# Optimization experiments

Measured on AMD Instinct MI355X. Metric: run time of the kernel, lower is better.

## Reference

```python
import math
import jax, jax.numpy as jnp
import numpy as np

W_BITS = 8
A_BITS = 8
N_HEADS = 16

def fake_quant(x, bits):
    # symmetric per-tensor fake quantization with straight-through estimator
    if bits >= 32:
        return x
    qmax = float(2 ** (bits - 1) - 1)
    scale = jnp.maximum(jnp.max(jnp.abs(x)) / qmax, 1e-8)
    q = jnp.round(x / scale) * scale
    return x + jax.lax.stop_gradient(q - x)

def qlinear(x, W, b):
    # QuantizeLinear: quantize activations (a_bits) and weights (w_bits), then y = x @ W^T + b
    xq = fake_quant(x, A_BITS)
    Wq = fake_quant(W, W_BITS)
    return jnp.einsum('bsd,ed->bse', xq, Wq) + b

def setup_inputs() -> dict:
    key = jax.random.key(0)
    B, S, D = 2, 2048, 1024
    ks = jax.random.split(key, 6)
    inp = {
        'hidden_states': jax.random.normal(ks[0], (B, S, D), dtype=jnp.float32),
        'attention_mask': jnp.ones((B, S), dtype=jnp.float32),
        'Wq': 0.02 * jax.random.normal(ks[1], (D, D), dtype=jnp.float32),
        'bq': jnp.zeros((D,), dtype=jnp.float32),
        'Wk': 0.02 * jax.random.normal(ks[2], (D, D), dtype=jnp.float32),
        'bk': jnp.zeros((D,), dtype=jnp.float32),
        'Wv': 0.02 * jax.random.normal(ks[3], (D, D), dtype=jnp.float32),
        'bv': jnp.zeros((D,), dtype=jnp.float32),
        'Wo': 0.02 * jax.random.normal(ks[4], (D, D), dtype=jnp.float32),
        'bo': jnp.zeros((D,), dtype=jnp.float32),
    }
    return inp

def reference(hidden_states, attention_mask, Wq, bq, Wk, bk, Wv, bv, Wo, bo):
    B, S, D = hidden_states.shape
    H = N_HEADS
    hd = D // H

    q = qlinear(hidden_states, Wq, bq).reshape(B, S, H, hd)
    k = qlinear(hidden_states, Wk, bk).reshape(B, S, H, hd)
    v = qlinear(hidden_states, Wv, bv).reshape(B, S, H, hd)

    # scores: [B, H, Sq, Sk]
    scores = jnp.einsum('bqhd,bkhd->bhqk', q, k) / math.sqrt(hd)
    mask_bias = (1.0 - attention_mask)[:, None, None, :] * -10000.0
    scores = scores + mask_bias
    probs = jax.nn.softmax(scores, axis=-1)

    attn = jnp.einsum('bhqk,bkhd->bqhd', probs, v).reshape(B, S, D)
    return qlinear(attn, Wo, bo)
```

## Files before the change

### kernel.cpp

```cpp
#include <hip/hip_runtime.h>
#include <cstddef>
#include <cstdint>

constexpr int Bb = 2, Ss = 2048, Dd = 1024, Hh = 16, HD = 64;
constexpr int Mm = Bb * Ss;

typedef int v4i __attribute__((ext_vector_type(4)));
typedef __bf16 bf16x8 __attribute__((ext_vector_type(8)));
typedef float f32x16 __attribute__((ext_vector_type(16)));

#define QPOSTMUL 0.18033688f
#define MASKBIAS -14426.950408f

__device__ __forceinline__ float qscale(float amax) {
    return fmaxf(amax / 127.0f, 1e-8f);
}

__device__ __forceinline__ unsigned short bf16rtn(float x) {
    __bf16 b = (__bf16)x;
    return __builtin_bit_cast(unsigned short, b);
}

__device__ __forceinline__ unsigned pack_bf16x2(float a, float b) {
    unsigned ua = __float_as_uint(a), ub = __float_as_uint(b);
    unsigned ha = (ua + 0x7fffu + ((ua >> 16) & 1u)) >> 16;
    unsigned hb = (ub + 0x7fffu + ((ub >> 16) & 1u)) & 0xffff0000u;
    return ha | hb;
}

__global__ void amax_all(const float4* __restrict__ hidden,
                         const float4* __restrict__ w0, const float4* __restrict__ w1,
                         const float4* __restrict__ w2, const float4* __restrict__ w3,
                         unsigned* __restrict__ slots) {
    const float4* src; int n4, slot, bx, nb;
    if (blockIdx.x < 448) { src = hidden; n4 = Mm * Dd / 4; slot = 0; bx = blockIdx.x; nb = 448; }
    else {
        int w = (blockIdx.x - 448) >> 4; bx = (blockIdx.x - 448) & 15; nb = 16;
        src = w == 0 ? w0 : w == 1 ? w1 : w == 2 ? w2 : w3;
        n4 = Dd * Dd / 4; slot = 1 + w;
    }
    float m = 0.f;
    for (int i = bx * blockDim.x + threadIdx.x; i < n4; i += nb * blockDim.x) {
        float4 v = src[i];
        m = fmaxf(m, fmaxf(fmaxf(fabsf(v.x), fabsf(v.y)), fmaxf(fabsf(v.z), fabsf(v.w))));
    }
    #pragma unroll
    for (int off = 32; off > 0; off >>= 1) m = fmaxf(m, __shfl_down(m, off, 64));
    __shared__ float sm[4];
    int lane = threadIdx.x & 63, wid = threadIdx.x >> 6;
    if (lane == 0) sm[wid] = m;
    __syncthreads();
    if (threadIdx.x == 0) {
        float mm = fmaxf(fmaxf(sm[0], sm[1]), fmaxf(sm[2], sm[3]));
        atomicMax(slots + slot, __float_as_uint(mm));
    }
}

__global__ void quant_all(const float* __restrict__ hidden,
                          const float* __restrict__ w0, const float* __restrict__ w1,
                          const float* __restrict__ w2, const float* __restrict__ w3,
                          const float* __restrict__ amax,
                          char* __restrict__ hq8, char* __restrict__ Wall8) {
    const float* x; char* y; int n4, slot, bx, nb;
    if (blockIdx.x < 1024) { x = hidden; y = hq8; n4 = Mm * Dd / 4; slot = 0; bx = blockIdx.x; nb = 1024; }
    else {
        int w = (blockIdx.x - 1024) >> 5; bx = (blockIdx.x - 1024) & 31; nb = 32;
        x = w == 0 ? w0 : w == 1 ? w1 : w == 2 ? w2 : w3;
        y = Wall8 + ((size_t)w << 20);
        n4 = Dd * Dd / 4; slot = 1 + w;
    }
    float s = qscale(amax[slot]);
    const float4* x4 = (const float4*)x;
    char4* y4 = (char4*)y;
    for (int i = bx * blockDim.x + threadIdx.x; i < n4; i += nb * blockDim.x) {
        float4 v = x4[i];
        char4 q;
        q.x = (char)(int)rintf(v.x / s);
        q.y = (char)(int)rintf(v.y / s);
        q.z = (char)(int)rintf(v.z / s);
        q.w = (char)(int)rintf(v.w / s);
        y4[i] = q;
    }
}

__global__ void quant_a(const float* __restrict__ x, char* __restrict__ y,
                        const float* __restrict__ amax, int n4) {
    float s = qscale(amax[0]);
    int stride = gridDim.x * blockDim.x;
    const float4* x4 = (const float4*)x;
    char4* y4 = (char4*)y;
    for (int i = blockIdx.x * blockDim.x + threadIdx.x; i < n4; i += stride) {
        float4 v = x4[i];
        char4 q;
        q.x = (char)(int)rintf(v.x / s);
        q.y = (char)(int)rintf(v.y / s);
        q.z = (char)(int)rintf(v.z / s);
        q.w = (char)(int)rintf(v.w / s);
        y4[i] = q;
    }
}

#define GLOAD_LDS16(g, l) __builtin_amdgcn_global_load_lds( \
    (const __attribute__((address_space(1))) unsigned int*)(g), \
    (__attribute__((address_space(3))) unsigned int*)(l), 16, 0, 0)

__device__ __forceinline__ void gemm128_core(const char* __restrict__ A, const char* __restrict__ Bw,
                                             int bm, int bn, int K, int t,
                                             char* At, char* Bt, v4i acc[4][4]) {
    const int lane = t & 63, w = t >> 6;
    const int wm = (w >> 1) * 64, wn = (w & 1) * 64;
    const int lr = lane & 15, kq = lane >> 4;
    const int rs = w * 16 + (lane >> 2);
    const int cc = lane & 3;

    for (int k0 = 0; k0 < K; k0 += 64) {
        __syncthreads();
        #pragma unroll
        for (int h = 0; h < 2; h++) {
            int r = rs + h * 64;
            int cs = cc ^ ((r >> 1) & 3);
            GLOAD_LDS16(A  + (size_t)(bm + r) * K + k0 + cs * 16, At + r * 64 + cc * 16);
            GLOAD_LDS16(Bw + (size_t)(bn + r) * K + k0 + cs * 16, Bt + r * 64 + cc * 16);
        }
        __syncthreads();

        v4i af[4], bf[4];
        #pragma unroll
        for (int mt = 0; mt < 4; mt++) {
            int row = wm + mt * 16 + lr;
            af[mt] = *(const v4i*)(At + row * 64 + ((kq ^ ((row >> 1) & 3)) << 4));
        }
        #pragma unroll
        for (int nt = 0; nt < 4; nt++) {
            int row = wn + nt * 16 + lr;
            bf[nt] = *(const v4i*)(Bt + row * 64 + ((kq ^ ((row >> 1) & 3)) << 4));
        }
        #pragma unroll
        for (int mt = 0; mt < 4; mt++)
            #pragma unroll
            for (int nt = 0; nt < 4; nt++)
                acc[mt][nt] = __builtin_amdgcn_mfma_i32_16x16x64_i8(af[mt], bf[nt], acc[mt][nt], 0, 0, 0);
    }
}

__global__ __launch_bounds__(256) void gemm_qkv(const char* __restrict__ A,
                                                const char* __restrict__ Wall8,
                                                const float* __restrict__ bq,
                                                const float* __restrict__ bk,
                                                const float* __restrict__ bv,
                                                const float* __restrict__ amax,
                                                unsigned short* __restrict__ qb16,
                                                unsigned short* __restrict__ kb16,
                                                unsigned short* __restrict__ vt16) {
    __shared__ alignas(16) char At[128 * 64];
    __shared__ alignas(16) char Bt[128 * 64];
    const int t = threadIdx.x, lane = t & 63, w = t >> 6;
    const int mat = blockIdx.x >> 3;
    const int bn = (blockIdx.x & 7) * 128, bm = blockIdx.y * 128;
    const int wm = (w >> 1) * 64, wn = (w & 1) * 64;
    const int lr = lane & 15, kq = lane >> 4;

    const v4i vzero = {0, 0, 0, 0};
    v4i acc[4][4];
    #pragma unroll
    for (int mt = 0; mt < 4; mt++)
        #pragma unroll
        for (int nt = 0; nt < 4; nt++) acc[mt][nt] = vzero;

    const char* Bw = Wall8 + ((size_t)mat << 20);
    gemm128_core(A, Bw, bm, bn, Dd, t, At, Bt, acc);

    const float* bias = mat == 0 ? bq : mat == 1 ? bk : bv;
    float sc = qscale(amax[0]) * qscale(amax[1 + mat]);
    float pm = (mat == 0) ? QPOSTMUL : 1.0f;

    #pragma unroll
    for (int nt = 0; nt < 4; nt++) {
        int n = bn + wn + nt * 16 + lr;
        float bv_ = bias[n];
        #pragma unroll
        for (int mt = 0; mt < 4; mt++) {
            if (mat == 2) {
                int m0 = bm + wm + mt * 16 + kq * 4;
                int b_ = m0 >> 11, s_ = m0 & 2047;
                int e = n & 63, hc = n >> 6;
                ushort4 hv;
                hv.x = bf16rtn((float)acc[mt][nt][0] * sc + bv_);
                hv.y = bf16rtn((float)acc[mt][nt][1] * sc + bv_);
                hv.z = bf16rtn((float)acc[mt][nt][2] * sc + bv_);
                hv.w = bf16rtn((float)acc[mt][nt][3] * sc + bv_);
                size_t ad = (((size_t)(b_ * Hh + hc) * 64 + e) * Ss) + s_;
                *(ushort4*)(vt16 + ad) = hv;
            } else {
                unsigned short* C = mat == 0 ? qb16 : kb16;
                #pragma unroll
                for (int rg = 0; rg < 4; rg++) {
                    int m = bm + wm + mt * 16 + kq * 4 + rg;
                    C[(size_t)m * Dd + n] = bf16rtn(((float)acc[mt][nt][rg] * sc + bv_) * pm);
                }
            }
        }
    }
}

__global__ __launch_bounds__(256) void gemm_o(const char* __restrict__ A,
                                              const char* __restrict__ Bw,
                                              const float* __restrict__ bias,
                                              const float* __restrict__ amaxA,
                                              const float* __restrict__ amaxB,
                                              float* __restrict__ C) {
    __shared__ alignas(16) char At[128 * 64];
    __shared__ alignas(16) char Bt[64 * 64];
    const int t = threadIdx.x, lane = t & 63, w = t >> 6;
    const int bn = blockIdx.x * 64, bm = blockIdx.y * 128;
    const int wm = (w >> 1) * 64, wn = (w & 1) * 32;
    const int lr = lane & 15, kq = lane >> 4;
    const int rs = t >> 2, cc = t & 3;
    const int cs = cc ^ ((rs >> 1) & 3);
    const int rs2 = rs + 64, cs2 = cc ^ ((rs2 >> 1) & 3);

    const v4i vzero = {0, 0, 0, 0};
    v4i acc[4][2];
    #pragma unroll
    for (int mt = 0; mt < 4; mt++) { acc[mt][0] = vzero; acc[mt][1] = vzero; }

    for (int k0 = 0; k0 < Dd; k0 += 64) {
        __syncthreads();
        GLOAD_LDS16(A  + (size_t)(bm + rs)  * Dd + k0 + cs  * 16, At + rs  * 64 + cc * 16);
        GLOAD_LDS16(A  + (size_t)(bm + rs2) * Dd + k0 + cs2 * 16, At + rs2 * 64 + cc * 16);
        GLOAD_LDS16(Bw + (size_t)(bn + rs)  * Dd + k0 + cs  * 16, Bt + rs  * 64 + cc * 16);
        __syncthreads();

        v4i af[4], bf[2];
        #pragma unroll
        for (int mt = 0; mt < 4; mt++) {
            int row = wm + mt * 16 + lr;
            af[mt] = *(const v4i*)(At + row * 64 + ((kq ^ ((row >> 1) & 3)) << 4));
        }
        #pragma unroll
        for (int nt = 0; nt < 2; nt++) {
            int row = wn + nt * 16 + lr;
            bf[nt] = *(const v4i*)(Bt + row * 64 + ((kq ^ ((row >> 1) & 3)) << 4));
        }
        #pragma unroll
        for (int mt = 0; mt < 4; mt++)
            #pragma unroll
            for (int nt = 0; nt < 2; nt++)
                acc[mt][nt] = __builtin_amdgcn_mfma_i32_16x16x64_i8(af[mt], bf[nt], acc[mt][nt], 0, 0, 0);
    }

    float sc = qscale(amaxA[0]) * qscale(amaxB[0]);
    #pragma unroll
    for (int nt = 0; nt < 2; nt++) {
        int n = bn + wn + nt * 16 + lr;
        float bv_ = bias[n];
        #pragma unroll
        for (int mt = 0; mt < 4; mt++)
            #pragma unroll
            for (int rg = 0; rg < 4; rg++) {
                int m = bm + wm + mt * 16 + kq * 4 + rg;
                C[(size_t)m * Dd + n] = (float)acc[mt][nt][rg] * sc + bv_;
            }
    }
}

__global__ __launch_bounds__(256) void attn_mfma(
    const unsigned short* __restrict__ qb16, const unsigned short* __restrict__ kb16,
    const unsigned short* __restrict__ vt16,
    const float* __restrict__ mask, float* __restrict__ Ob, unsigned* __restrict__ amax_out) {
    __shared__ alignas(16) unsigned short KsHi[64][72], VsHi[64][72];
    __shared__ alignas(16) unsigned PwU[4][32][36];
    __shared__ float mbias[64];
    __shared__ float wred[4];

    const int t = threadIdx.x, lane = t & 63, wq = t >> 6;
    const int ln31 = lane & 31, h5 = lane >> 5;
    const int b = blockIdx.z, h = blockIdx.y, q0 = blockIdx.x * 128;

    bf16x8 qf[4];
    {
        int qrow = q0 + wq * 32 + ln31;
        const unsigned short* qb_ = qb16 + ((size_t)(b * Ss + qrow)) * Dd + h * 64 + h5 * 8;
        #pragma unroll
        for (int c = 0; c < 4; c++) qf[c] = *(const bf16x8*)(qb_ + c * 16);
    }

    const int srow = t >> 2, cp = (t & 3) * 2;
    const int rho = (srow >> 1) + (srow & 1) * 32;
    int4 pk0, pk1, pv0, pv1; float pmask = 1.f;
    auto prefetch = [&](int k0) {
        const unsigned short* gk = kb16 + ((size_t)(b * Ss + k0 + srow)) * Dd + h * 64 + cp * 8;
        const unsigned short* gv = vt16 + (((size_t)(b * Hh + h) * 64 + srow)) * Ss + k0 + cp * 8;
        pk0 = *(const int4*)gk; pk1 = *(const int4*)(gk + 8);
        pv0 = *(const int4*)gv; pv1 = *(const int4*)(gv + 8);
        if (t < 64) pmask = mask[b * Ss + k0 + t];
    };

    f32x16 o0 = 0.f, o1 = 0.f;
    float lp[16];
    #pragma unroll
    for (int r = 0; r < 16; r++) lp[r] = 0.f;

    prefetch(0);
    for (int k0 = 0; k0 < Ss; k0 += 64) {
        __syncthreads();
        *(int4*)&KsHi[rho][cp * 8]      = pk0;
        *(int4*)&KsHi[rho][cp * 8 + 8]  = pk1;
        *(int4*)&VsHi[srow][cp * 8]     = pv0;
        *(int4*)&VsHi[srow][cp * 8 + 8] = pv1;
        if (t < 64) mbias[t] = (1.0f - pmask) * MASKBIAS;
        __syncthreads();
        if (k0 + 64 < Ss) prefetch(k0 + 64);

        f32x16 sc0 = 0.f, sc1 = 0.f;
        #pragma unroll
        for (int c = 0; c < 4; c++) {
            bf16x8 kh0 = *(const bf16x8*)&KsHi[ln31][c * 16 + h5 * 8];
            bf16x8 kh1 = *(const bf16x8*)&KsHi[32 + ln31][c * 16 + h5 * 8];
            sc0 = __builtin_amdgcn_mfma_f32_32x32x16_bf16(qf[c], kh0, sc0, 0, 0, 0);
            sc1 = __builtin_amdgcn_mfma_f32_32x32x16_bf16(qf[c], kh1, sc1, 0, 0, 0);
        }

        float mb0 = mbias[2 * ln31], mb1 = mbias[2 * ln31 + 1];
        #pragma unroll
        for (int r = 0; r < 16; r++) {
            float p0 = __builtin_amdgcn_exp2f(sc0[r] + mb0);
            float p1 = __builtin_amdgcn_exp2f(sc1[r] + mb1);
            lp[r] += p0 + p1;
            int row = (r & 3) + 8 * (r >> 2) + 4 * h5;
            PwU[wq][row][ln31] = pack_bf16x2(p0, p1);
        }

        #pragma unroll
        for (int c = 0; c < 4; c++) {
            bf16x8 pf = *(const bf16x8*)((const unsigned short*)&PwU[wq][ln31][0] + c * 16 + h5 * 8);
            bf16x8 vh0 = *(const bf16x8*)&VsHi[ln31][c * 16 + h5 * 8];
            bf16x8 vh1 = *(const bf16x8*)&VsHi[32 + ln31][c * 16 + h5 * 8];
            o0 = __builtin_amdgcn_mfma_f32_32x32x16_bf16(pf, vh0, o0, 0, 0, 0);
            o1 = __builtin_amdgcn_mfma_f32_32x32x16_bf16(pf, vh1, o1, 0, 0, 0);
        }
    }

    float lmax = 0.f;
    #pragma unroll
    for (int r = 0; r < 16; r++) {
        float l = lp[r];
        #pragma unroll
        for (int off = 1; off < 32; off <<= 1) l += __shfl_xor(l, off, 32);
        float inv = 1.0f / l;
        int row = q0 + wq * 32 + (r & 3) + 8 * (r >> 2) + 4 * h5;
        size_t ro = ((size_t)(b * Ss + row)) * Dd + h * 64;
        float v0 = o0[r] * inv, v1 = o1[r] * inv;
        Ob[ro + ln31] = v0;
        Ob[ro + 32 + ln31] = v1;
        lmax = fmaxf(lmax, fmaxf(fabsf(v0), fabsf(v1)));
    }
    #pragma unroll
    for (int off = 32; off > 0; off >>= 1) lmax = fmaxf(lmax, __shfl_xor(lmax, off, 64));
    if (lane == 0) wred[wq] = lmax;
    __syncthreads();
    if (t == 0) {
        float m = fmaxf(fmaxf(wred[0], wred[1]), fmaxf(wred[2], wred[3]));
        atomicMax(amax_out, __float_as_uint(m));
    }
}

extern "C" void kernel_launch(void* const* d_in, const int* in_sizes, int n_in,
                              void* d_out, int out_size, void* d_ws, size_t ws_size,
                              hipStream_t stream) {
    const float* hidden = (const float*)d_in[0];
    const float* mask   = (const float*)d_in[1];
    const float* Wq = (const float*)d_in[2];
    const float* bq = (const float*)d_in[3];
    const float* Wk = (const float*)d_in[4];
    const float* bk = (const float*)d_in[5];
    const float* Wv = (const float*)d_in[6];
    const float* bv = (const float*)d_in[7];
    const float* Wo = (const float*)d_in[8];
    const float* bo = (const float*)d_in[9];
    float* out = (float*)d_out;

    char* ws = (char*)d_ws;
    float* scal = (float*)ws;
    size_t off = 1024;
    const size_t szH8 = (size_t)Mm * Dd;
    const size_t szHb = (size_t)Mm * Dd * sizeof(unsigned short);
    const size_t szHf = (size_t)Mm * Dd * sizeof(float);
    char* hq8   = ws + off; off += szH8;
    char* Wall8 = ws + off; off += 4u << 20;
    char* aq8   = ws + off; off += szH8;
    unsigned short* qb16 = (unsigned short*)(ws + off); off += szHb;
    unsigned short* kb16 = (unsigned short*)(ws + off); off += szHb;
    unsigned short* vt16 = (unsigned short*)(ws + off); off += szHb;
    float* ab = (float*)(ws + off); off += szHf;

    hipMemsetAsync(scal, 0, 64, stream);

    amax_all<<<512, 256, 0, stream>>>((const float4*)hidden, (const float4*)Wq,
                                      (const float4*)Wk, (const float4*)Wv, (const float4*)Wo,
                                      (unsigned*)scal);
    quant_all<<<1152, 256, 0, stream>>>(hidden, Wq, Wk, Wv, Wo, scal, hq8, Wall8);

    gemm_qkv<<<dim3(24, 32), 256, 0, stream>>>(hq8, Wall8, bq, bk, bv, scal,
                                               qb16, kb16, vt16);

    attn_mfma<<<dim3(Ss / 128, Hh, Bb), 256, 0, stream>>>(qb16, kb16, vt16,
                                                          mask, ab, (unsigned*)(scal + 5));

    quant_a<<<1024, 256, 0, stream>>>(ab, aq8, scal + 5, Mm * Dd / 4);

    gemm_o<<<dim3(16, 32), 256, 0, stream>>>(aq8, Wall8 + (3u << 20), bo,
                                             scal + 5, scal + 4, out);
}
```

Measured before the change: 237.8 us.

## Split attention key blocks across wave pairs with 64-query tiles and LDS reduction

The attention kernel now handles 64 queries per block instead of 128. Each pair of waves shares a 32-query slice and splits every 64-key tile in half, and their partial outputs and row sums are combined through a shared-memory buffer at the end. This doubles the grid size to raise occupancy and parallelism, and halves per-wave MFMA work per tile. In exchange, K/V tiles are loaded from global memory twice as often per query, and a final cross-wave reduction plus extra syncs are added. Shared memory is pooled and aliased so the reduction buffer reuses the K/V/P space.

```diff
diff --git a/kernel.cpp b/kernel.cpp
--- a/kernel.cpp
+++ b/kernel.cpp
@@ -19,13 +19,6 @@
 __device__ __forceinline__ unsigned short bf16rtn(float x) {
     __bf16 b = (__bf16)x;
     return __builtin_bit_cast(unsigned short, b);
-}
-
-__device__ __forceinline__ unsigned pack_bf16x2(float a, float b) {
-    unsigned ua = __float_as_uint(a), ub = __float_as_uint(b);
-    unsigned ha = (ua + 0x7fffu + ((ua >> 16) & 1u)) >> 16;
-    unsigned hb = (ub + 0x7fffu + ((ub >> 16) & 1u)) & 0xffff0000u;
-    return ha | hb;
 }
 
 __global__ void amax_all(const float4* __restrict__ hidden,
@@ -268,25 +261,29 @@
     const unsigned short* __restrict__ qb16, const unsigned short* __restrict__ kb16,
     const unsigned short* __restrict__ vt16,
     const float* __restrict__ mask, float* __restrict__ Ob, unsigned* __restrict__ amax_out) {
-    __shared__ alignas(16) unsigned short KsHi[64][72], VsHi[64][72];
-    __shared__ alignas(16) unsigned PwU[4][32][36];
-    __shared__ float mbias[64];
-    __shared__ float wred[4];
+    __shared__ alignas(16) char pool[27904];
+    unsigned short (*Ks)[72] = (unsigned short(*)[72])(pool);
+    unsigned short (*Vs)[72] = (unsigned short(*)[72])(pool + 9216);
+    unsigned short (*Pw)[32][72] = (unsigned short(*)[32][72])(pool + 18432);
+    float* mbias = (float*)(pool + 27648);
+    float (*Obuf)[32][68] = (float(*)[32][68])(pool);
+    __shared__ float lred[2][2][32];
+    __shared__ float wred[2];
 
     const int t = threadIdx.x, lane = t & 63, wq = t >> 6;
     const int ln31 = lane & 31, h5 = lane >> 5;
-    const int b = blockIdx.z, h = blockIdx.y, q0 = blockIdx.x * 128;
+    const int qsub = wq >> 1, khalf = wq & 1;
+    const int b = blockIdx.z, h = blockIdx.y, q0 = blockIdx.x * 64;
 
     bf16x8 qf[4];
     {
-        int qrow = q0 + wq * 32 + ln31;
+        int qrow = q0 + qsub * 32 + ln31;
         const unsigned short* qb_ = qb16 + ((size_t)(b * Ss + qrow)) * Dd + h * 64 + h5 * 8;
         #pragma unroll
         for (int c = 0; c < 4; c++) qf[c] = *(const bf16x8*)(qb_ + c * 16);
     }
 
     const int srow = t >> 2, cp = (t & 3) * 2;
-    const int rho = (srow >> 1) + (srow & 1) * 32;
     int4 pk0, pk1, pv0, pv1; float pmask = 1.f;
     auto prefetch = [&](int k0) {
         const unsigned short* gk = kb16 + ((size_t)(b * Ss + k0 + srow)) * Dd + h * 64 + cp * 8;
@@ -304,65 +301,77 @@
     prefetch(0);
     for (int k0 = 0; k0 < Ss; k0 += 64) {
         __syncthreads();
-        *(int4*)&KsHi[rho][cp * 8]      = pk0;
-        *(int4*)&KsHi[rho][cp * 8 + 8]  = pk1;
-        *(int4*)&VsHi[srow][cp * 8]     = pv0;
-        *(int4*)&VsHi[srow][cp * 8 + 8] = pv1;
+        *(int4*)&Ks[srow][cp * 8]     = pk0;
+        *(int4*)&Ks[srow][cp * 8 + 8] = pk1;
+        *(int4*)&Vs[srow][cp * 8]     = pv0;
+        *(int4*)&Vs[srow][cp * 8 + 8] = pv1;
         if (t < 64) mbias[t] = (1.0f - pmask) * MASKBIAS;
         __syncthreads();
         if (k0 + 64 < Ss) prefetch(k0 + 64);
 
-        f32x16 sc0 = 0.f, sc1 = 0.f;
+        const int kb = khalf * 32;
+        float mbK = mbias[kb + ln31];
+        f32x16 sc = 0.f;
         #pragma unroll
         for (int c = 0; c < 4; c++) {
-            bf16x8 kh0 = *(const bf16x8*)&KsHi[ln31][c * 16 + h5 * 8];
-            bf16x8 kh1 = *(const bf16x8*)&KsHi[32 + ln31][c * 16 + h5 * 8];
-            sc0 = __builtin_amdgcn_mfma_f32_32x32x16_bf16(qf[c], kh0, sc0, 0, 0, 0);
-            sc1 = __builtin_amdgcn_mfma_f32_32x32x16_bf16(qf[c], kh1, sc1, 0, 0, 0);
-        }
-
-        float mb0 = mbias[2 * ln31], mb1 = mbias[2 * ln31 + 1];
+            bf16x8 kh = *(const bf16x8*)&Ks[kb + ln31][c * 16 + h5 * 8];
+            sc = __builtin_amdgcn_mfma_f32_32x32x16_bf16(qf[c], kh, sc, 0, 0, 0);
+        }
+
         #pragma unroll
         for (int r = 0; r < 16; r++) {
-            float p0 = __builtin_amdgcn_exp2f(sc0[r] + mb0);
-            float p1 = __builtin_amdgcn_exp2f(sc1[r] + mb1);
-            lp[r] += p0 + p1;
+            float p = __builtin_amdgcn_exp2f(sc[r] + mbK);
+            lp[r] += p;
             int row = (r & 3) + 8 * (r >> 2) + 4 * h5;
-            PwU[wq][row][ln31] = pack_bf16x2(p0, p1);
-        }
-
-        #pragma unroll
-        for (int c = 0; c < 4; c++) {
-            bf16x8 pf = *(const bf16x8*)((const unsigned short*)&PwU[wq][ln31][0] + c * 16 + h5 * 8);
-            bf16x8 vh0 = *(const bf16x8*)&VsHi[ln31][c * 16 + h5 * 8];
-            bf16x8 vh1 = *(const bf16x8*)&VsHi[32 + ln31][c * 16 + h5 * 8];
+            Pw[qsub][row][kb + ln31] = bf16rtn(p);
+        }
+
+        #pragma unroll
+        for (int c = 0; c < 2; c++) {
+            bf16x8 pf  = *(const bf16x8*)&Pw[qsub][ln31][kb + c * 16 + h5 * 8];
+            bf16x8 vh0 = *(const bf16x8*)&Vs[ln31][kb + c * 16 + h5 * 8];
+            bf16x8 vh1 = *(const bf16x8*)&Vs[32 + ln31][kb + c * 16 + h5 * 8];
             o0 = __builtin_amdgcn_mfma_f32_32x32x16_bf16(pf, vh0, o0, 0, 0, 0);
             o1 = __builtin_amdgcn_mfma_f32_32x32x16_bf16(pf, vh1, o1, 0, 0, 0);
         }
     }
 
-    float lmax = 0.f;
+    __syncthreads();
     #pragma unroll
     for (int r = 0; r < 16; r++) {
         float l = lp[r];
         #pragma unroll
         for (int off = 1; off < 32; off <<= 1) l += __shfl_xor(l, off, 32);
-        float inv = 1.0f / l;
-        int row = q0 + wq * 32 + (r & 3) + 8 * (r >> 2) + 4 * h5;
-        size_t ro = ((size_t)(b * Ss + row)) * Dd + h * 64;
-        float v0 = o0[r] * inv, v1 = o1[r] * inv;
-        Ob[ro + ln31] = v0;
-        Ob[ro + 32 + ln31] = v1;
-        lmax = fmaxf(lmax, fmaxf(fabsf(v0), fabsf(v1)));
-    }
-    #pragma unroll
-    for (int off = 32; off > 0; off >>= 1) lmax = fmaxf(lmax, __shfl_xor(lmax, off, 64));
-    if (lane == 0) wred[wq] = lmax;
+        if (ln31 == 0) lred[qsub][khalf][(r & 3) + 8 * (r >> 2) + 4 * h5] = l;
+    }
+    if (khalf == 1) {
+        #pragma unroll
+        for (int r = 0; r < 16; r++) {
+            int row = (r & 3) + 8 * (r >> 2) + 4 * h5;
+            Obuf[qsub][row][ln31] = o0[r];
+            Obuf[qsub][row][32 + ln31] = o1[r];
+        }
+    }
     __syncthreads();
-    if (t == 0) {
-        float m = fmaxf(fmaxf(wred[0], wred[1]), fmaxf(wred[2], wred[3]));
-        atomicMax(amax_out, __float_as_uint(m));
-    }
+    if (khalf == 0) {
+        float lmax = 0.f;
+        #pragma unroll
+        for (int r = 0; r < 16; r++) {
+            int row = (r & 3) + 8 * (r >> 2) + 4 * h5;
+            float inv = 1.0f / (lred[qsub][0][row] + lred[qsub][1][row]);
+            float v0 = (o0[r] + Obuf[qsub][row][ln31]) * inv;
+            float v1 = (o1[r] + Obuf[qsub][row][32 + ln31]) * inv;
+            size_t ro = ((size_t)(b * Ss + q0 + qsub * 32 + row)) * Dd + h * 64;
+            Ob[ro + ln31] = v0;
+            Ob[ro + 32 + ln31] = v1;
+            lmax = fmaxf(lmax, fmaxf(fabsf(v0), fabsf(v1)));
+        }
+        #pragma unroll
+        for (int off = 32; off > 0; off >>= 1) lmax = fmaxf(lmax, __shfl_xor(lmax, off, 64));
+        if (lane == 0) wred[qsub] = lmax;
+    }
+    __syncthreads();
+    if (t == 0) atomicMax(amax_out, __float_as_uint(fmaxf(wred[0], wred[1])));
 }
 
 extern "C" void kernel_launch(void* const* d_in, const int* in_sizes, int n_in,
@@ -404,8 +413,8 @@
     gemm_qkv<<<dim3(24, 32), 256, 0, stream>>>(hq8, Wall8, bq, bk, bv, scal,
                                                qb16, kb16, vt16);
 
-    attn_mfma<<<dim3(Ss / 128, Hh, Bb), 256, 0, stream>>>(qb16, kb16, vt16,
-                                                          mask, ab, (unsigned*)(scal + 5));
+    attn_mfma<<<dim3(Ss / 64, Hh, Bb), 256, 0, stream>>>(qb16, kb16, vt16,
+                                                         mask, ab, (unsigned*)(scal + 5));
 
     quant_a<<<1024, 256, 0, stream>>>(ab, aq8, scal + 5, Mm * Dd / 4);
 
```

Result: slower. 243.5 us (+2.4%).

## Load K/V fragments directly from global into registers, dropping shared staging

Applied to the files above, without the earlier changes.

The attention kernel no longer stages K and V tiles through shared memory with two block barriers per step. Each lane now loads its MFMA fragments for K, V and the mask straight from global memory into double-buffered registers, prefetching the next 64-key tile while the current one is computed. This removes LDS traffic and __syncthreads, but raises register pressure and means each wave fetches the full K/V tiles independently, relying on cache for reuse across the four waves. The bf16 packing helper is also switched to compiler conversions.

```diff
diff --git a/kernel.cpp b/kernel.cpp
--- a/kernel.cpp
+++ b/kernel.cpp
@@ -7,6 +7,7 @@
 
 typedef int v4i __attribute__((ext_vector_type(4)));
 typedef __bf16 bf16x8 __attribute__((ext_vector_type(8)));
+typedef __bf16 bf16x2 __attribute__((ext_vector_type(2)));
 typedef float f32x16 __attribute__((ext_vector_type(16)));
 
 #define QPOSTMUL 0.18033688f
@@ -22,10 +23,10 @@
 }
 
 __device__ __forceinline__ unsigned pack_bf16x2(float a, float b) {
-    unsigned ua = __float_as_uint(a), ub = __float_as_uint(b);
-    unsigned ha = (ua + 0x7fffu + ((ua >> 16) & 1u)) >> 16;
-    unsigned hb = (ub + 0x7fffu + ((ub >> 16) & 1u)) & 0xffff0000u;
-    return ha | hb;
+    bf16x2 v;
+    v[0] = (__bf16)a;
+    v[1] = (__bf16)b;
+    return __builtin_bit_cast(unsigned, v);
 }
 
 __global__ void amax_all(const float4* __restrict__ hidden,
@@ -268,9 +269,7 @@
     const unsigned short* __restrict__ qb16, const unsigned short* __restrict__ kb16,
     const unsigned short* __restrict__ vt16,
     const float* __restrict__ mask, float* __restrict__ Ob, unsigned* __restrict__ amax_out) {
-    __shared__ alignas(16) unsigned short KsHi[64][72], VsHi[64][72];
     __shared__ alignas(16) unsigned PwU[4][32][36];
-    __shared__ float mbias[64];
     __shared__ float wred[4];
 
     const int t = threadIdx.x, lane = t & 63, wq = t >> 6;
@@ -285,43 +284,45 @@
         for (int c = 0; c < 4; c++) qf[c] = *(const bf16x8*)(qb_ + c * 16);
     }
 
-    const int srow = t >> 2, cp = (t & 3) * 2;
-    const int rho = (srow >> 1) + (srow & 1) * 32;
-    int4 pk0, pk1, pv0, pv1; float pmask = 1.f;
-    auto prefetch = [&](int k0) {
-        const unsigned short* gk = kb16 + ((size_t)(b * Ss + k0 + srow)) * Dd + h * 64 + cp * 8;
-        const unsigned short* gv = vt16 + (((size_t)(b * Hh + h) * 64 + srow)) * Ss + k0 + cp * 8;
-        pk0 = *(const int4*)gk; pk1 = *(const int4*)(gk + 8);
-        pv0 = *(const int4*)gv; pv1 = *(const int4*)(gv + 8);
-        if (t < 64) pmask = mask[b * Ss + k0 + t];
-    };
+    const unsigned short* kbase = kb16 + ((size_t)(b * Ss)) * Dd + h * 64 + h5 * 8;
+    const unsigned short* vbase = vt16 + ((size_t)(b * Hh + h) * 64) * Ss + h5 * 8;
+    const float* mbase = mask + b * Ss;
 
     f32x16 o0 = 0.f, o1 = 0.f;
     float lp[16];
     #pragma unroll
     for (int r = 0; r < 16; r++) lp[r] = 0.f;
 
-    prefetch(0);
-    for (int k0 = 0; k0 < Ss; k0 += 64) {
-        __syncthreads();
-        *(int4*)&KsHi[rho][cp * 8]      = pk0;
-        *(int4*)&KsHi[rho][cp * 8 + 8]  = pk1;
-        *(int4*)&VsHi[srow][cp * 8]     = pv0;
-        *(int4*)&VsHi[srow][cp * 8 + 8] = pv1;
-        if (t < 64) mbias[t] = (1.0f - pmask) * MASKBIAS;
-        __syncthreads();
-        if (k0 + 64 < Ss) prefetch(k0 + 64);
+    bf16x8 kf[2][8], vf[2][8];
+    float mk[2][2];
+    auto loadf = [&](int s, int k0) {
+        const unsigned short* ke = kbase + (size_t)(k0 + 2 * ln31) * Dd;
+        const unsigned short* ko = ke + Dd;
+        const unsigned short* v0 = vbase + (size_t)ln31 * Ss + k0;
+        const unsigned short* v1 = vbase + (size_t)(32 + ln31) * Ss + k0;
+        #pragma unroll
+        for (int c = 0; c < 4; c++) {
+            kf[s][c]     = *(const bf16x8*)(ke + c * 16);
+            kf[s][4 + c] = *(const bf16x8*)(ko + c * 16);
+            vf[s][c]     = *(const bf16x8*)(v0 + c * 16);
+            vf[s][4 + c] = *(const bf16x8*)(v1 + c * 16);
+        }
+        mk[s][0] = mbase[k0 + 2 * ln31];
+        mk[s][1] = mbase[k0 + 2 * ln31 + 1];
+    };
+
+    auto body = [&](int s, int ns, int k0) {
+        if (k0 + 64 < Ss) loadf(ns, k0 + 64);
 
         f32x16 sc0 = 0.f, sc1 = 0.f;
         #pragma unroll
         for (int c = 0; c < 4; c++) {
-            bf16x8 kh0 = *(const bf16x8*)&KsHi[ln31][c * 16 + h5 * 8];
-            bf16x8 kh1 = *(const bf16x8*)&KsHi[32 + ln31][c * 16 + h5 * 8];
-            sc0 = __builtin_amdgcn_mfma_f32_32x32x16_bf16(qf[c], kh0, sc0, 0, 0, 0);
-            sc1 = __builtin_amdgcn_mfma_f32_32x32x16_bf16(qf[c], kh1, sc1, 0, 0, 0);
-        }
-
-        float mb0 = mbias[2 * ln31], mb1 = mbias[2 * ln31 + 1];
+            sc0 = __builtin_amdgcn_mfma_f32_32x32x16_bf16(qf[c], kf[s][c], sc0, 0, 0, 0);
+            sc1 = __builtin_amdgcn_mfma_f32_32x32x16_bf16(qf[c], kf[s][4 + c], sc1, 0, 0, 0);
+        }
+
+        float mb0 = (1.0f - mk[s][0]) * MASKBIAS;
+        float mb1 = (1.0f - mk[s][1]) * MASKBIAS;
         #pragma unroll
         for (int r = 0; r < 16; r++) {
             float p0 = __builtin_amdgcn_exp2f(sc0[r] + mb0);
@@ -334,11 +335,15 @@
         #pragma unroll
         for (int c = 0; c < 4; c++) {
             bf16x8 pf = *(const bf16x8*)((const unsigned short*)&PwU[wq][ln31][0] + c * 16 + h5 * 8);
-            bf16x8 vh0 = *(const bf16x8*)&VsHi[ln31][c * 16 + h5 * 8];
-            bf16x8 vh1 = *(const bf16x8*)&VsHi[32 + ln31][c * 16 + h5 * 8];
-            o0 = __builtin_amdgcn_mfma_f32_32x32x16_bf16(pf, vh0, o0, 0, 0, 0);
-            o1 = __builtin_amdgcn_mfma_f32_32x32x16_bf16(pf, vh1, o1, 0, 0, 0);
-        }
+            o0 = __builtin_amdgcn_mfma_f32_32x32x16_bf16(pf, vf[s][c], o0, 0, 0, 0);
+            o1 = __builtin_amdgcn_mfma_f32_32x32x16_bf16(pf, vf[s][4 + c], o1, 0, 0, 0);
+        }
+    };
+
+    loadf(0, 0);
+    for (int k0 = 0; k0 < Ss; k0 += 128) {
+        body(0, 1, k0);
+        body(1, 0, k0 + 64);
     }
 
     float lmax = 0.f;
```

After: 313.4 us. 31.8% more time.
